# Kernel optimization log

Hardware: AMD Instinct MI355X
Metric: run time of the kernel (lower is better)

## Reference

```python
import jax, jax.numpy as jnp
import numpy as np

B, N_PATTS, D_PATTS, L_PATTS, L_SEQ = 32, 32, 12, 32, 1024
L_OUT = 32
RHO = 1.0
BIG = 1e30  # stands in for +inf at DP boundaries (finite to keep grads clean)


def setup_inputs() -> dict:
    key = jax.random.key(0)
    kx, kp = jax.random.split(key)
    x = jax.random.normal(kx, (B, D_PATTS, L_SEQ), dtype=jnp.float32)
    patts = jax.random.normal(kp, (N_PATTS, D_PATTS, L_PATTS), dtype=jnp.float32)
    return {"x": x, "patts": patts}


def _pairwise_sqdist(x, patts):
    # cost[b,n,i,j] = sum_d (patts[n,d,i] - x[b,d,j])^2, shape [B,N,P,L]
    x2 = jnp.sum(x * x, axis=1)            # [B,L]
    p2 = jnp.sum(patts * patts, axis=1)    # [N,P]
    cross = jnp.einsum('bdl,ndp->bnpl', x, patts)  # [B,N,P,L]
    return p2[None, :, :, None] + x2[:, None, None, :] - 2.0 * cross


def _dp_column(a, c, w):
    # Solve cur[i] = c[i] + min(a[i], w*cur[i-1]) sequentially over pattern axis.
    # a, c: [B,N,P]; returns [B,N,P]
    a_t = jnp.moveaxis(a, -1, 0)  # [P,B,N]
    c_t = jnp.moveaxis(c, -1, 0)

    def step(cur_prev, ac):
        a_i, c_i = ac
        cur = c_i + jnp.minimum(a_i, w * cur_prev)
        return cur, cur

    init = jnp.full(c.shape[:-1], BIG, c.dtype)  # no row above the first
    _, cur = jax.lax.scan(step, init, (a_t, c_t))
    return jnp.moveaxis(cur, 0, -1)


def _dtw_dp(cost, w):
    # Weighted DTW recurrence:
    #   D[i,j] = cost[i,j] + min(D[i-1,j-1], w*D[i-1,j], w*D[i,j-1])
    # with D[0,0] = cost[0,0] and out-of-range predecessors = +inf.
    # cost: [B,N,P,L] -> D: [B,N,P,L]
    Bb, Nn, P, L = cost.shape
    cost_t = jnp.moveaxis(cost, -1, 0)  # [L,B,N,P]

    # first column j=0: D[i,0] = c[i,0] + w*D[i-1,0], D[0,0] = c[0,0]
    a0 = jnp.where(jnp.arange(P) == 0, 0.0, BIG).astype(cost.dtype)
    a0 = jnp.broadcast_to(a0, cost.shape[:3])
    d0 = _dp_column(a0, cost_t[0], w)  # [B,N,P]

    def outer_step(d_prev, c_col):
        # prev_shift[i] = D[i-1, j-1]; boundary row is +inf for j >= 1
        top = jnp.full_like(d_prev[..., :1], BIG)
        prev_shift = jnp.concatenate([top, d_prev[..., :-1]], axis=-1)
        a = jnp.minimum(prev_shift, w * d_prev)
        cur = _dp_column(a, c_col, w)
        return cur, cur

    _, rest = jax.lax.scan(outer_step, d0, cost_t[1:])  # [L-1,B,N,P]
    D = jnp.concatenate([d0[None], rest], axis=0)       # [L,B,N,P]
    return jnp.moveaxis(D, 0, -1)                       # [B,N,P,L]


def reference(x, patts):
    w = RHO ** (1.0 / L_PATTS)
    cost = _pairwise_sqdist(x, patts)   # [B,N,P,L]
    D = _dtw_dp(cost, w)                # [B,N,P,L]
    return D[..., -L_OUT:]              # [B,N,P,L_OUT]
```

## Files before the change

### kernel.cpp

```cpp
#include <hip/hip_runtime.h>


#define BIGF 1e30f
#define LL   1024
#define LOUT 32

using v4f = __attribute__((ext_vector_type(4))) float;

template<int CTRL>
__device__ __forceinline__ float dpp_self(float v) {
    return __int_as_float(__builtin_amdgcn_update_dpp(
        __float_as_int(v), __float_as_int(v), CTRL, 0xF, 0xF, false));
}
__device__ __forceinline__ float wshr1z(float v) {
    return __int_as_float(__builtin_amdgcn_update_dpp(
        0, __float_as_int(v), 0x138 , 0xF, 0xF, false));
}
__device__ __forceinline__ float rdlane(float v, int l) {
    return __int_as_float(__builtin_amdgcn_readlane(__float_as_int(v), l));
}

__device__ __forceinline__ float scan_min64_fast(float t, int lane) {
    t = fminf(t, dpp_self<0x111>(t));
    t = fminf(t, dpp_self<0x112>(t));
    t = fminf(t, dpp_self<0x114>(t));
    t = fminf(t, dpp_self<0x118>(t));
    float r0 = rdlane(t, 15), r1 = rdlane(t, 31), r2 = rdlane(t, 47);
    t = fminf(t, (lane >= 16) ? r0 : BIGF);
    t = fminf(t, (lane >= 32) ? r1 : BIGF);
    t = fminf(t, (lane >= 48) ? r2 : BIGF);
    return t;
}

__device__ __forceinline__ float scan_add64(float t, int lane) {
#pragma unroll
    for (int d = 1; d < 64; d <<= 1) {
        float o = __shfl_up(t, (unsigned)d, 64);
        t += (lane >= d) ? o : 0.0f;
    }
    return t;
}

__global__ __launch_bounds__(64)
__attribute__((amdgpu_waves_per_eu(1, 1)))
void dtw_kernel(const float* __restrict__ x, const float* __restrict__ patts,
                float* __restrict__ out) {
    __shared__ float pT[32 * 12];
    __shared__ float p2s[32];

    const int lane = threadIdx.x;
    const bool l0  = (lane == 0);
    const int blk  = blockIdx.x;
    const int b    = blk >> 5, n = blk & 31;
    const float* __restrict__ xb = x + b * (12 * LL);
    const float* __restrict__ pn = patts + n * (12 * 32);

    if (lane < 32) {
        float s2 = 0.f;
#pragma unroll
        for (int d = 0; d < 12; ++d) {
            float v = pn[d * 32 + lane];
            s2 = fmaf(v, v, s2);
            pT[lane * 12 + d] = -2.0f * v;
        }
        p2s[lane] = s2;
    }

    float SX[12][16];
#pragma unroll
    for (int d = 0; d < 12; ++d) {
#pragma unroll
        for (int c = 0; c < 4; ++c) {
            v4f v = *(const v4f*)(xb + d * LL + 16 * lane + 4 * c);
            SX[d][4*c+0] = v.x; SX[d][4*c+1] = v.y;
            SX[d][4*c+2] = v.z; SX[d][4*c+3] = v.w;
        }
    }
    float SX2[16];
#pragma unroll
    for (int k = 0; k < 16; ++k) {
        float a = 0.f;
#pragma unroll
        for (int d = 0; d < 12; ++d) a = fmaf(SX[d][k], SX[d][k], a);
        SX2[k] = a;
    }
#pragma unroll
    for (int d = 0; d < 12; ++d) {
#pragma unroll
        for (int k = 1; k < 16; ++k) SX[d][k] += SX[d][k-1];
        float tot = SX[d][15];
        float ex  = scan_add64(tot, lane) - tot;
#pragma unroll
        for (int k = 0; k < 16; ++k) SX[d][k] += ex;
    }
    {
#pragma unroll
        for (int k = 1; k < 16; ++k) SX2[k] += SX2[k-1];
        float tot = SX2[15];
        float ex  = scan_add64(tot, lane) - tot;
#pragma unroll
        for (int k = 0; k < 16; ++k) SX2[k] += ex;
    }
    float jp1[16];
#pragma unroll
    for (int k = 0; k < 16; ++k) jp1[k] = (float)(16 * lane + k + 1);

    __syncthreads();

    float pv[12], p2u;
#pragma unroll
    for (int d = 0; d < 12; ++d) pv[d] = pT[d];
    p2u = p2s[0];

    float S[16], Dp[16];
#pragma unroll
    for (int k = 0; k < 16; ++k) S[k] = fmaf(p2u, jp1[k], SX2[k]);
#pragma unroll
    for (int d = 0; d < 12; ++d)
#pragma unroll
        for (int k = 0; k < 16; ++k) S[k] = fmaf(pv[d], SX[d][k], S[k]);
#pragma unroll
    for (int k = 0; k < 16; ++k) Dp[k] = S[k];
    if (lane >= 62) {
        float* ob = out + blk * (32 * LOUT) + (lane - 62) * 16;
#pragma unroll
        for (int c = 0; c < 4; ++c) {
            v4f v = {Dp[4*c], Dp[4*c+1], Dp[4*c+2], Dp[4*c+3]};
            *(v4f*)(ob + 4 * c) = v;
        }
    }

#pragma unroll
    for (int d = 0; d < 12; ++d) pv[d] = pT[12 + d];
    p2u = p2s[1];
#pragma unroll
    for (int k = 0; k < 16; ++k) S[k] = fmaf(p2u, jp1[k], SX2[k]);
#pragma unroll
    for (int d = 0; d < 12; ++d)
#pragma unroll
        for (int k = 0; k < 16; ++k) S[k] = fmaf(pv[d], SX[d][k], S[k]);

#pragma unroll 1
    for (int i = 1; i < 32; ++i) {
        const int ip = (i + 1 < 32) ? i + 1 : 31;
        float pvn[12];
#pragma unroll
        for (int d = 0; d < 12; ++d) pvn[d] = pT[ip * 12 + d];
        float p2n = p2s[ip];

        float dsh = wshr1z(Dp[15]); dsh = l0 ? BIGF : dsh;
        float se  = wshr1z(S[15]);

        float m[16];
        m[0] = fminf(dsh, Dp[0]) - se;
#pragma unroll
        for (int k = 1; k < 16; ++k)
            m[k] = fminf(m[k-1], fminf(Dp[k-1], Dp[k]) - S[k-1]);

        float t = scan_min64_fast(m[15], lane);

        float Sn[16];
#pragma unroll
        for (int k = 0; k < 16; ++k) Sn[k] = fmaf(p2n, jp1[k], SX2[k]);
#pragma unroll
        for (int d = 0; d < 12; ++d)
#pragma unroll
            for (int k = 0; k < 16; ++k) Sn[k] = fmaf(pvn[d], SX[d][k], Sn[k]);

        float te = wshr1z(t); te = l0 ? BIGF : te;
#pragma unroll
        for (int k = 0; k < 16; ++k) Dp[k] = S[k] + fminf(te, m[k]);

        if (lane >= 62) {
            float* ob = out + blk * (32 * LOUT) + (lane - 62) * 16;
#pragma unroll
            for (int c = 0; c < 4; ++c) {
                v4f v = {Dp[4*c], Dp[4*c+1], Dp[4*c+2], Dp[4*c+3]};
                *(v4f*)(ob + i * 32 + 4 * c) = v;
            }
        }
#pragma unroll
        for (int k = 0; k < 16; ++k) S[k] = Sn[k];
    }
}

extern "C" void kernel_launch(void* const* d_in, const int* in_sizes, int n_in,
                              void* d_out, int out_size, void* d_ws, size_t ws_size,
                              hipStream_t stream) {
    const float* x     = (const float*)d_in[0];
    const float* patts = (const float*)d_in[1];
    float* out         = (float*)d_out;
    dtw_kernel<<<dim3(1024), dim3(64), 0, stream>>>(x, patts, out);
}
```

Before: 82.08 us.

## Keep pattern rows in registers via readlane and drop software-pipelined cost row

Pattern coefficients now stay in per-lane registers and are broadcast with readlane, so the shared-memory staging and the __syncthreads barrier are gone. The cost row for each pattern index is computed inside the loop right before it is used, rather than one iteration ahead. This frees the Sn registers and removes LDS loads, but the cost FMAs can no longer overlap the latency of the cross-lane min-scan.

```diff
diff --git a/kernel.cpp b/kernel.cpp
--- a/kernel.cpp
+++ b/kernel.cpp
@@ -31,7 +31,6 @@
     t = fminf(t, (lane >= 48) ? r2 : BIGF);
     return t;
 }
-
 __device__ __forceinline__ float scan_add64(float t, int lane) {
 #pragma unroll
     for (int d = 1; d < 64; d <<= 1) {
@@ -45,9 +44,6 @@
 __attribute__((amdgpu_waves_per_eu(1, 1)))
 void dtw_kernel(const float* __restrict__ x, const float* __restrict__ patts,
                 float* __restrict__ out) {
-    __shared__ float pT[32 * 12];
-    __shared__ float p2s[32];
-
     const int lane = threadIdx.x;
     const bool l0  = (lane == 0);
     const int blk  = blockIdx.x;
@@ -55,15 +51,17 @@
     const float* __restrict__ xb = x + b * (12 * LL);
     const float* __restrict__ pn = patts + n * (12 * 32);
 
-    if (lane < 32) {
+    float prm[12], p2r;
+    {
+        const int r = lane & 31;
         float s2 = 0.f;
 #pragma unroll
         for (int d = 0; d < 12; ++d) {
-            float v = pn[d * 32 + lane];
+            float v = pn[d * 32 + r];
             s2 = fmaf(v, v, s2);
-            pT[lane * 12 + d] = -2.0f * v;
+            prm[d] = -2.0f * v;
         }
-        p2s[lane] = s2;
+        p2r = s2;
     }
 
     float SX[12][16];
@@ -105,48 +103,43 @@
 #pragma unroll
     for (int k = 0; k < 16; ++k) jp1[k] = (float)(16 * lane + k + 1);
 
-    __syncthreads();
-
-    float pv[12], p2u;
+    float S[16], Dp[16];
+    {
+        float pv[12], p2u;
 #pragma unroll
-    for (int d = 0; d < 12; ++d) pv[d] = pT[d];
-    p2u = p2s[0];
-
-    float S[16], Dp[16];
+        for (int d = 0; d < 12; ++d) pv[d] = rdlane(prm[d], 0);
+        p2u = rdlane(p2r, 0);
 #pragma unroll
-    for (int k = 0; k < 16; ++k) S[k] = fmaf(p2u, jp1[k], SX2[k]);
+        for (int k = 0; k < 16; ++k) S[k] = fmaf(p2u, jp1[k], SX2[k]);
 #pragma unroll
-    for (int d = 0; d < 12; ++d)
+        for (int d = 0; d < 12; ++d)
 #pragma unroll
-        for (int k = 0; k < 16; ++k) S[k] = fmaf(pv[d], SX[d][k], S[k]);
+            for (int k = 0; k < 16; ++k) S[k] = fmaf(pv[d], SX[d][k], S[k]);
 #pragma unroll
-    for (int k = 0; k < 16; ++k) Dp[k] = S[k];
-    if (lane >= 62) {
-        float* ob = out + blk * (32 * LOUT) + (lane - 62) * 16;
+        for (int k = 0; k < 16; ++k) Dp[k] = S[k];
+        if (lane >= 62) {
+            float* ob = out + blk * (32 * LOUT) + (lane - 62) * 16;
 #pragma unroll
-        for (int c = 0; c < 4; ++c) {
-            v4f v = {Dp[4*c], Dp[4*c+1], Dp[4*c+2], Dp[4*c+3]};
-            *(v4f*)(ob + 4 * c) = v;
+            for (int c = 0; c < 4; ++c) {
+                v4f v = {Dp[4*c], Dp[4*c+1], Dp[4*c+2], Dp[4*c+3]};
+                *(v4f*)(ob + 4 * c) = v;
+            }
         }
     }
 
-#pragma unroll
-    for (int d = 0; d < 12; ++d) pv[d] = pT[12 + d];
-    p2u = p2s[1];
-#pragma unroll
-    for (int k = 0; k < 16; ++k) S[k] = fmaf(p2u, jp1[k], SX2[k]);
-#pragma unroll
-    for (int d = 0; d < 12; ++d)
-#pragma unroll
-        for (int k = 0; k < 16; ++k) S[k] = fmaf(pv[d], SX[d][k], S[k]);
-
 #pragma unroll 1
     for (int i = 1; i < 32; ++i) {
-        const int ip = (i + 1 < 32) ? i + 1 : 31;
-        float pvn[12];
+        float pv[12], p2u;
 #pragma unroll
-        for (int d = 0; d < 12; ++d) pvn[d] = pT[ip * 12 + d];
-        float p2n = p2s[ip];
+        for (int d = 0; d < 12; ++d) pv[d] = rdlane(prm[d], i);
+        p2u = rdlane(p2r, i);
+
+#pragma unroll
+        for (int k = 0; k < 16; ++k) S[k] = fmaf(p2u, jp1[k], SX2[k]);
+#pragma unroll
+        for (int d = 0; d < 12; ++d)
+#pragma unroll
+            for (int k = 0; k < 16; ++k) S[k] = fmaf(pv[d], SX[d][k], S[k]);
 
         float dsh = wshr1z(Dp[15]); dsh = l0 ? BIGF : dsh;
         float se  = wshr1z(S[15]);
@@ -157,17 +150,9 @@
         for (int k = 1; k < 16; ++k)
             m[k] = fminf(m[k-1], fminf(Dp[k-1], Dp[k]) - S[k-1]);
 
-        float t = scan_min64_fast(m[15], lane);
+        float t  = scan_min64_fast(m[15], lane);
+        float te = wshr1z(t); te = l0 ? BIGF : te;
 
-        float Sn[16];
-#pragma unroll
-        for (int k = 0; k < 16; ++k) Sn[k] = fmaf(p2n, jp1[k], SX2[k]);
-#pragma unroll
-        for (int d = 0; d < 12; ++d)
-#pragma unroll
-            for (int k = 0; k < 16; ++k) Sn[k] = fmaf(pvn[d], SX[d][k], Sn[k]);
-
-        float te = wshr1z(t); te = l0 ? BIGF : te;
 #pragma unroll
         for (int k = 0; k < 16; ++k) Dp[k] = S[k] + fminf(te, m[k]);
 
@@ -179,8 +164,6 @@
                 *(v4f*)(ob + i * 32 + 4 * c) = v;
             }
         }
-#pragma unroll
-        for (int k = 0; k < 16; ++k) S[k] = Sn[k];
     }
 }
 
```

Measured after the change: 80.31 us. 2.2% less time.
